# Performance work log

Hardware: AMD Instinct MI355X
Metric: run time of the kernel (lower is better)

Reference implementation:

```python
import jax, jax.numpy as jnp
import numpy as np

N, E, G, B, L = 24576, 98304, 512, 512, 1000
F_IN, H1, C1, C2, HID = 5, 2, 64, 128, 256


def setup_inputs() -> dict:
    key = jax.random.key(0)
    ks = jax.random.split(key, 20)
    rn = lambda k, s: jax.random.normal(k, s, jnp.float32) * 0.1
    return {
        "x": jax.random.normal(ks[0], (N, F_IN), jnp.float32),
        "edge_index": jax.random.randint(ks[1], (2, E), 0, N),
        "batch": jnp.sort(jax.random.randint(ks[2], (N,), 0, G)),
        "protein_seq": jax.random.randint(ks[3], (B, L), 0, 22),
        "W1": rn(ks[4], (F_IN, H1 * C1)), "att_src1": rn(ks[5], (H1, C1)), "att_dst1": rn(ks[6], (H1, C1)), "b1": jnp.zeros((H1 * C1,), jnp.float32),
        "W2": rn(ks[7], (H1 * C1, C2)), "att_src2": rn(ks[8], (1, C2)), "att_dst2": rn(ks[9], (1, C2)), "b2": jnp.zeros((C2,), jnp.float32),
        "Wd": rn(ks[10], (C2, HID)), "bd": jnp.zeros((HID,), jnp.float32),
        "Pe": rn(ks[11], (22, 64)),
        "K1": rn(ks[12], (64, 64, 3)), "bk1": jnp.zeros((64,), jnp.float32),
        "K2": rn(ks[13], (128, 64, 5)), "bk2": jnp.zeros((128,), jnp.float32),
        "Wp": rn(ks[14], (128, HID)), "bp": jnp.zeros((HID,), jnp.float32),
        "Wf1": rn(ks[15], (2 * HID, 128)), "bf1": jnp.zeros((128,), jnp.float32),
        "Wf2": rn(ks[16], (128, 64)), "bf2": jnp.zeros((64,), jnp.float32),
        "Wo": rn(ks[17], (64, 1)), "bo": jnp.zeros((1,), jnp.float32),
    }


def _gat(x, edge_index, W, att_src, att_dst, b, heads, out_ch):
    """PyG GATConv: add self-loops, per-edge LeakyReLU(0.2) scores, segment softmax over dst."""
    n = x.shape[0]
    h = (x @ W).reshape(n, heads, out_ch)
    loop = jnp.arange(n)
    src = jnp.concatenate([edge_index[0], loop])
    dst = jnp.concatenate([edge_index[1], loop])
    a_s = jnp.sum(h * att_src[None], axis=-1)  # [n, H]
    a_d = jnp.sum(h * att_dst[None], axis=-1)
    e = jax.nn.leaky_relu(a_s[src] + a_d[dst], negative_slope=0.2)  # [E+n, H]
    m = jax.ops.segment_max(e, dst, num_segments=n)
    w = jnp.exp(e - m[dst])
    den = jax.ops.segment_sum(w, dst, num_segments=n)
    alpha = w / (den[dst] + 1e-16)
    out = jax.ops.segment_sum(h[src] * alpha[..., None], dst, num_segments=n)
    return out.reshape(n, heads * out_ch) + b


def _conv1d(x, k, pad):  # x: [B,C,L], k: [O,I,K]
    return jax.lax.conv_general_dilated(x, k, (1,), [(pad, pad)], dimension_numbers=("NCH", "OIH", "NCH"))


def reference(x, edge_index, batch, protein_seq, W1, att_src1, att_dst1, b1, W2, att_src2, att_dst2, b2, Wd, bd, Pe, K1, bk1, K2, bk2, Wp, bp, Wf1, bf1, Wf2, bf2, Wo, bo):
    # drug branch (GAT x2 + global mean pool)
    g = jax.nn.elu(_gat(x, edge_index, W1, att_src1, att_dst1, b1, H1, C1))
    g = jax.nn.elu(_gat(g, edge_index, W2, att_src2, att_dst2, b2, 1, C2))
    sums = jax.ops.segment_sum(g, batch, num_segments=G)
    cnt = jax.ops.segment_sum(jnp.ones((g.shape[0], 1), g.dtype), batch, num_segments=G)
    drug = jax.nn.relu(sums / jnp.maximum(cnt, 1.0) @ Wd + bd)
    # protein branch (embed -> conv1d x2 -> global max pool)
    pe = Pe[protein_seq].transpose(0, 2, 1)  # [B, 64, L]
    p = jax.nn.elu(_conv1d(pe, K1, 1) + bk1[None, :, None])
    p = jax.nn.elu(_conv1d(p, K2, 2) + bk2[None, :, None])
    prot = jax.nn.relu(jnp.max(p, axis=2) @ Wp + bp)
    # head
    h = jnp.concatenate([drug, prot], axis=1)
    h = jax.nn.relu(h @ Wf1 + bf1)
    h = jax.nn.relu(h @ Wf2 + bf2)
    return h @ Wo + bo
```

## Files before the change

### kernel.cpp

```cpp
#include <hip/hip_runtime.h>
#include <hip/hip_bf16.h>
#include <math.h>

#define NN 24576
#define NE 98304
#define ETOT (NE + NN)
#define NG 512
#define NB 512
#define LL 1000
#define TL 124
#define NTILE 9
#define PROT_BLKS (NB * NTILE)
#define CNT_BLKS (ETOT / 256)
#define AS1_BLKS (NN * 2 / 256)

typedef __attribute__((ext_vector_type(8))) short short8;
typedef __attribute__((ext_vector_type(4))) short short4v;
typedef __attribute__((ext_vector_type(4))) float f32x4;

__device__ inline short f2bf(float x) {
    union { __hip_bfloat16 b; short s; } u;
    u.b = __float2bfloat16(x);
    return u.s;
}

__device__ inline float bf2f(short s) {
    return __uint_as_float(((unsigned)(unsigned short)s) << 16);
}

__device__ inline void atomicMaxFloat(float* addr, float val) {
    int* ai = (int*)addr;
    int old = __float_as_int(*addr);
    while (__int_as_float(old) < val) {
        int assumed = old;
        old = atomicCAS(ai, assumed, __float_as_int(val));
        if (old == assumed) break;
    }
}

__global__ void k_init_prep(int* deg, int* cursor, float* sums, float* cnt, float* pmax,
                            const float* K1, const float* K2, const float* W2, const float* Pe,
                            const float* W1, const float* as1c, const float* ad1c,
                            const float* as2c, const float* ad2c,
                            short* Bswz1, short* Bswz2, short* Bh2, short* Bl2, short* Peb,
                            float* wvec) {
    int bid = blockIdx.x, t = threadIdx.x;
    if (bid < 256) {
        int i = bid * 256 + t;
        if (i < NN) { deg[i] = 0; cursor[i] = 0; }
        if (i < NG * 128) sums[i] = 0.f;
        if (i < NG) cnt[i] = 0.f;
        if (i < NB * 128) pmax[i] = -1e30f;
        return;
    }
    int idx = (bid - 256) * 256 + t;
    if (idx < 22 * 64) Peb[idx] = f2bf(Pe[idx]);
    if (idx < 20) {
        int q = idx % 10, hd = q / 5, f = q % 5;
        const float* av = (idx < 10) ? as1c : ad1c;
        float s = 0.f;
        for (int c = 0; c < 64; c++) s += W1[f * 128 + hd * 64 + c] * av[hd * 64 + c];
        wvec[idx < 10 ? q : 10 + q] = s;
    }
    if (idx >= 32 && idx < 288) {
        int q = idx - 32;
        int kk = q & 127;
        const float* av = (q < 128) ? as2c : ad2c;
        float s = 0.f;
        for (int n2 = 0; n2 < 128; n2++) s += W2[kk * 128 + n2] * av[n2];
        wvec[idx] = s;
    }
    if (idx < 192 * 64) {
        int j = idx & 7, lane = (idx >> 3) & 63, rest = idx >> 9;
        int nt = rest & 3, kb = rest >> 2;
        int k = kb * 32 + ((lane >> 4) << 3) + j;
        int n = nt * 16 + (lane & 15);
        int kk = k >> 6, i = k & 63;
        Bswz1[idx] = f2bf(K1[n * 192 + i * 3 + kk]);
    }
    if (idx < 320 * 128) {
        int j = idx & 7, lane = (idx >> 3) & 63, rest = idx >> 9;
        int nt = rest & 7, kb = rest >> 3;
        int k = kb * 32 + ((lane >> 4) << 3) + j;
        int n = nt * 16 + (lane & 15);
        int kk = k / 64, i = k % 64;
        Bswz2[idx] = f2bf(K2[n * 320 + i * 5 + kk]);
    }
    if (idx < 128 * 128) {
        int j = idx & 7, lane = (idx >> 3) & 63, rest = idx >> 9;
        int nt = rest & 7, kb = rest >> 3;
        int k = kb * 32 + ((lane >> 4) << 3) + j;
        int n = nt * 16 + (lane & 15);
        float v = W2[k * 128 + n];
        short hh = f2bf(v);
        Bh2[idx] = hh;
        Bl2[idx] = f2bf(v - bf2f(hh));
    }
}

#define SSTR 72
__global__ __launch_bounds__(256, 4) void k_prot_cnt_as1(
    const int* seq, const short* Peb, const short* Bswz1, const float* bk1,
    const short* Bswz2, const float* bk2, float* pmax,
    const int* ei, int* deg,
    const float* x, const float* wvec, float* as1o, float* ad1o) {
    int bid = blockIdx.x;
    int t = threadIdx.x;

    if (bid >= PROT_BLKS) {
        int rb = bid - PROT_BLKS;
        if (rb < CNT_BLKS) {
            int e = rb * 256 + t;
            int d = (e < NE) ? ei[NE + e] : e - NE;
            atomicAdd(&deg[d], 1);
        } else {
            int idx = (rb - CNT_BLKS) * 256 + t;
            int n = idx >> 1, hd = idx & 1;
            float s = 0.f, dv = 0.f;
#pragma unroll
            for (int f = 0; f < 5; f++) {
                float xv = x[n * 5 + f];
                s += xv * wvec[hd * 5 + f];
                dv += xv * wvec[10 + hd * 5 + f];
            }
            as1o[idx] = s;
            ad1o[idx] = dv;
        }
        return;
    }

    __shared__ __align__(16) short sEmb[130 * SSTR];
    __shared__ __align__(16) short s1[132 * SSTR];

    int b = bid / NTILE;
    int tile = bid - b * NTILE;
    int t0 = tile * TL;
    int wv = t >> 6, lane = t & 63;
    int ln15 = lane & 15, quad = lane >> 4;
    int mhalf = wv & 1, nhalf = wv >> 1;

    for (int j0 = 0; j0 < 130; j0 += 64) {
        int j = j0 + (t >> 2);
        if (j < 130) {
            int c0 = (t & 3) * 16;
            int l = t0 - 3 + j;
            int id = (l >= 0 && l < LL) ? seq[b * LL + l] : -1;
            short* dst = &sEmb[j * SSTR + c0];
            if (id >= 0) {
                const short8* src = (const short8*)&Peb[id * 64 + c0];
                *(short8*)dst = src[0];
                *(short8*)(dst + 8) = src[1];
            } else {
                *(short8*)dst = (short8){0, 0, 0, 0, 0, 0, 0, 0};
                *(short8*)(dst + 8) = (short8){0, 0, 0, 0, 0, 0, 0, 0};
            }
        }
    }
    s1[(128 + (t >> 6)) * SSTR + (t & 63)] = 0;
    __syncthreads();

    {
        f32x4 acc[4][2];
#pragma unroll
        for (int mi = 0; mi < 4; mi++)
#pragma unroll
            for (int ni = 0; ni < 2; ni++) acc[mi][ni] = (f32x4){0.f, 0.f, 0.f, 0.f};
#pragma unroll
        for (int kb = 0; kb < 6; kb++) {
            int koff = kb * 32 + quad * 8;
            int kk = koff >> 6, i0 = koff & 63;
            short8 b0 = *(const short8*)&Bswz1[((kb * 4 + nhalf * 2 + 0) * 64 + lane) * 8];
            short8 b1 = *(const short8*)&Bswz1[((kb * 4 + nhalf * 2 + 1) * 64 + lane) * 8];
#pragma unroll
            for (int mi = 0; mi < 4; mi++) {
                int arow = (mhalf * 4 + mi) * 16 + ln15 + kk;
                short8 a = *(const short8*)&sEmb[arow * SSTR + i0];
                acc[mi][0] = __builtin_amdgcn_mfma_f32_16x16x32_bf16(a, b0, acc[mi][0], 0, 0, 0);
                acc[mi][1] = __builtin_amdgcn_mfma_f32_16x16x32_bf16(a, b1, acc[mi][1], 0, 0, 0);
            }
        }
#pragma unroll
        for (int mi = 0; mi < 4; mi++) {
            int mt = mhalf * 4 + mi;
#pragma unroll
            for (int ni = 0; ni < 2; ni++) {
                int col = (nhalf * 2 + ni) * 16 + ln15;
                float bias = bk1[col];
#pragma unroll
                for (int r = 0; r < 4; r++) {
                    int q = mt * 16 + quad * 4 + r;
                    int l = t0 - 2 + q;
                    float v = acc[mi][ni][r] + bias;
                    v = v > 0.f ? v : __expf(v) - 1.f;
                    s1[q * SSTR + col] = (l >= 0 && l < LL) ? f2bf(v) : (short)0;
                }
            }
        }
    }
    __syncthreads();

    f32x4 acc2[4][4];
#pragma unroll
    for (int mi = 0; mi < 4; mi++)
#pragma unroll
        for (int ni = 0; ni < 4; ni++) acc2[mi][ni] = (f32x4){0.f, 0.f, 0.f, 0.f};
#pragma unroll 2
    for (int kb = 0; kb < 10; kb++) {
        int koff = kb * 32 + quad * 8;
        int kk = koff >> 6, i0 = koff & 63;
        short8 a[4], bb[4];
#pragma unroll
        for (int mi = 0; mi < 4; mi++) {
            int arow = (mhalf * 4 + mi) * 16 + ln15 + kk;
            a[mi] = *(const short8*)&s1[arow * SSTR + i0];
        }
#pragma unroll
        for (int ni = 0; ni < 4; ni++)
            bb[ni] = *(const short8*)&Bswz2[((kb * 8 + nhalf * 4 + ni) * 64 + lane) * 8];
#pragma unroll
        for (int mi = 0; mi < 4; mi++)
#pragma unroll
            for (int ni = 0; ni < 4; ni++)
                acc2[mi][ni] = __builtin_amdgcn_mfma_f32_16x16x32_bf16(a[mi], bb[ni], acc2[mi][ni], 0, 0, 0);
    }

#pragma unroll
    for (int ni = 0; ni < 4; ni++) {
        int col = (nhalf * 4 + ni) * 16 + ln15;
        float mx = -1e30f;
#pragma unroll
        for (int mi = 0; mi < 4; mi++) {
#pragma unroll
            for (int r = 0; r < 4; r++) {
                int p = (mhalf * 4 + mi) * 16 + quad * 4 + r;
                if (p < TL && t0 + p < LL) mx = fmaxf(mx, acc2[mi][ni][r]);
            }
        }
        mx = fmaxf(mx, __shfl_xor(mx, 16, 64));
        mx = fmaxf(mx, __shfl_xor(mx, 32, 64));
        if (quad == 0) {
            float v = mx + bk2[col];
            v = v > 0.f ? v : __expf(v) - 1.f;
            atomicMaxFloat(&pmax[b * 128 + col], v);
        }
    }
}

__global__ void k_scan1(const int* deg, int* excl, int* part) {
    __shared__ int s[256];
    int b = blockIdx.x, t = threadIdx.x, i = b * 256 + t;
    int v = deg[i];
    s[t] = v;
    __syncthreads();
    for (int o = 1; o < 256; o <<= 1) {
        int x = (t >= o) ? s[t - o] : 0;
        __syncthreads();
        s[t] += x;
        __syncthreads();
    }
    excl[i] = s[t] - v;
    if (t == 255) part[b] = s[t];
}

__global__ void k_scan23(const int* excl, const int* part, int* rowptr) {
    __shared__ int sp[96];
    __shared__ int pref;
    int b = blockIdx.x, t = threadIdx.x;
    if (t < 96) sp[t] = part[t];
    __syncthreads();
    if (t == 0) {
        int run = 0;
        for (int i = 0; i < b; i++) run += sp[i];
        pref = run;
    }
    __syncthreads();
    int i = b * 256 + t;
    rowptr[i] = excl[i] + pref;
    if (i == 0) rowptr[NN] = ETOT;
}

__global__ void k_scatter(const int* ei, const int* rowptr, int* cursor, int* colidx) {
    int e = blockIdx.x * 256 + threadIdx.x;
    if (e >= ETOT) return;
    int s, d;
    if (e < NE) { s = ei[e]; d = ei[NE + e]; }
    else { s = d = e - NE; }
    int pos = atomicAdd(&cursor[d], 1);
    colidx[rowptr[d] + pos] = s;
}

__global__ void k_agg2x(const int* rowptr, const int* colidx, const float* x,
                        const float* as_, const float* ad_,
                        const float* W1, const float* b1, const float* wvec,
                        unsigned int* g1b, float* as2, float* ad2) {
    __shared__ float sW[640];
    __shared__ float sb1[128];
    __shared__ float swa[256];
    int t = threadIdx.x;
    for (int i = t; i < 640; i += 256) sW[i] = W1[i];
    if (t < 128) { sb1[t] = b1[t]; swa[t] = wvec[32 + t]; swa[128 + t] = wvec[160 + t]; }
    __syncthreads();

    int d = blockIdx.x * 16 + (t >> 4);
    int g = t & 15;
    int hd = (g < 5) ? 0 : 1;
    int f = (g < 5) ? g : g - 5;
    float adv = ad_[d * 2 + hd];
    int p0 = rowptr[d], p1 = rowptr[d + 1];
    float den = 0.f, acc = 0.f;
    if (g < 10) {
        for (int pc = p0; pc < p1; pc += 4) {
            int sarr[4]; float ev[4], xv[4];
#pragma unroll
            for (int i = 0; i < 4; i++) {
                int pp = pc + i;
                sarr[i] = colidx[pp < p1 ? pp : p1 - 1];
            }
#pragma unroll
            for (int i = 0; i < 4; i++) {
                ev[i] = as_[sarr[i] * 2 + hd];
                xv[i] = x[sarr[i] * 5 + f];
            }
#pragma unroll
            for (int i = 0; i < 4; i++) {
                if (pc + i < p1) {
                    float e = ev[i] + adv;
                    e = e >= 0.f ? e : 0.2f * e;
                    float w = __expf(e);
                    den += w;
                    acc += w * xv[i];
                }
            }
        }
    }
    float xn = acc / (den + 1e-16f);
    int gb = (t & 63) & ~15;
    int hcol = g >> 3;
    float xs[5];
#pragma unroll
    for (int f2 = 0; f2 < 5; f2++)
        xs[f2] = __shfl(xn, gb + hcol * 5 + f2, 64);
    float ps = 0.f, pd = 0.f;
    float g1v[8];
#pragma unroll
    for (int k = 0; k < 8; k++) {
        int col = g * 8 + k;
        float v = sb1[col];
#pragma unroll
        for (int f2 = 0; f2 < 5; f2++) v += xs[f2] * sW[f2 * 128 + col];
        v = v > 0.f ? v : __expf(v) - 1.f;
        g1v[k] = v;
        ps += v * swa[col];
        pd += v * swa[128 + col];
    }
    uint4 pk;
    pk.x = ((unsigned)(unsigned short)f2bf(g1v[1]) << 16) | (unsigned)(unsigned short)f2bf(g1v[0]);
    pk.y = ((unsigned)(unsigned short)f2bf(g1v[3]) << 16) | (unsigned)(unsigned short)f2bf(g1v[2]);
    pk.z = ((unsigned)(unsigned short)f2bf(g1v[5]) << 16) | (unsigned)(unsigned short)f2bf(g1v[4]);
    pk.w = ((unsigned)(unsigned short)f2bf(g1v[7]) << 16) | (unsigned)(unsigned short)f2bf(g1v[6]);
    *(uint4*)&g1b[d * 64 + g * 4] = pk;
#pragma unroll
    for (int msk = 1; msk < 16; msk <<= 1) {
        ps += __shfl_xor(ps, msk, 64);
        pd += __shfl_xor(pd, msk, 64);
    }
    if (g == 0) { as2[d] = ps; ad2[d] = pd; }
}

__global__ void k_agg1y(const int* rowptr, const int* colidx, const unsigned int* hb,
                        const float* as_, const float* ad_, float* yacc) {
    int t = threadIdx.x;
    int d = blockIdx.x * 4 + (t >> 6);
    int c = t & 63;
    float adv = ad_[d];
    int p0 = rowptr[d], p1 = rowptr[d + 1];
    float den = 0.f, acc0 = 0.f, acc1 = 0.f;
    for (int pc = p0; pc < p1; pc += 4) {
        int sarr[4]; float ev[4]; unsigned int hv[4];
#pragma unroll
        for (int i = 0; i < 4; i++) {
            int pp = pc + i;
            sarr[i] = colidx[pp < p1 ? pp : p1 - 1];
        }
#pragma unroll
        for (int i = 0; i < 4; i++) {
            ev[i] = as_[sarr[i]];
            hv[i] = hb[sarr[i] * 64 + c];
        }
#pragma unroll
        for (int i = 0; i < 4; i++) {
            if (pc + i < p1) {
                float e = ev[i] + adv;
                e = e >= 0.f ? e : 0.2f * e;
                float w = __expf(e);
                den += w;
                acc0 += w * __uint_as_float(hv[i] << 16);
                acc1 += w * __uint_as_float(hv[i] & 0xFFFF0000u);
            }
        }
    }
    float inv = 1.f / (den + 1e-16f);
    ((float2*)yacc)[d * 64 + c] = (float2){acc0 * inv, acc1 * inv};
}

#define ASTR 136
__global__ __launch_bounds__(256, 2) void k_g2mm(
    const float* yacc, const short* Bh, const short* Bl, const float* b2, float* g2) {
    __shared__ __align__(16) short Ah[64 * ASTR];
    __shared__ __align__(16) short Al[64 * ASTR];
    int t = threadIdx.x;
    int m0 = blockIdx.x * 64;
    int wv = t >> 6, lane = t & 63;
    int ln15 = lane & 15, quad = lane >> 4;

    for (int i = t; i < 64 * 32; i += 256) {
        int row = i >> 5, c4 = (i & 31) * 4;
        float4 v = *(const float4*)&yacc[(m0 + row) * 128 + c4];
        short4v hi, lo;
        hi.x = f2bf(v.x); lo.x = f2bf(v.x - bf2f(hi.x));
        hi.y = f2bf(v.y); lo.y = f2bf(v.y - bf2f(hi.y));
        hi.z = f2bf(v.z); lo.z = f2bf(v.z - bf2f(hi.z));
        hi.w = f2bf(v.w); lo.w = f2bf(v.w - bf2f(hi.w));
        *(short4v*)&Ah[row * ASTR + c4] = hi;
        *(short4v*)&Al[row * ASTR + c4] = lo;
    }
    __syncthreads();

    f32x4 acc[8];
#pragma unroll
    for (int nt = 0; nt < 8; nt++) acc[nt] = (f32x4){0.f, 0.f, 0.f, 0.f};
    int arow = wv * 16 + ln15;
#pragma unroll
    for (int kb = 0; kb < 4; kb++) {
        int koff = kb * 32 + quad * 8;
        short8 a_hi = *(const short8*)&Ah[arow * ASTR + koff];
        short8 a_lo = *(const short8*)&Al[arow * ASTR + koff];
#pragma unroll
        for (int nt = 0; nt < 8; nt++) {
            short8 bh = *(const short8*)&Bh[((kb * 8 + nt) * 64 + lane) * 8];
            short8 bl = *(const short8*)&Bl[((kb * 8 + nt) * 64 + lane) * 8];
            acc[nt] = __builtin_amdgcn_mfma_f32_16x16x32_bf16(a_hi, bh, acc[nt], 0, 0, 0);
            acc[nt] = __builtin_amdgcn_mfma_f32_16x16x32_bf16(a_hi, bl, acc[nt], 0, 0, 0);
            acc[nt] = __builtin_amdgcn_mfma_f32_16x16x32_bf16(a_lo, bh, acc[nt], 0, 0, 0);
        }
    }
#pragma unroll
    for (int nt = 0; nt < 8; nt++) {
        int col = nt * 16 + ln15;
        float bias = b2[col];
#pragma unroll
        for (int r = 0; r < 4; r++) {
            float v = acc[nt][r] + bias;
            v = v > 0.f ? v : __expf(v) - 1.f;
            int n = m0 + wv * 16 + quad * 4 + r;
            g2[n * 128 + col] = v;
        }
    }
}

__global__ void k_pool(const float* g2, const int* batch, float* sums, float* cnt) {
    __shared__ int sb[96];
    int blk = blockIdx.x, j = threadIdx.x;
    int n0 = blk * 96;
    if (j < 96) sb[j] = batch[n0 + j];
    __syncthreads();
    float v[4];
#pragma unroll
    for (int i = 0; i < 4; i++) v[i] = g2[(n0 + i) * 128 + j];
    int cur = sb[0], runStart = 0;
    float acc = 0.f;
    for (int q0 = 0; q0 < 96; q0 += 4) {
        float nv[4] = {0.f, 0.f, 0.f, 0.f};
        if (q0 + 4 < 96) {
#pragma unroll
            for (int i = 0; i < 4; i++) nv[i] = g2[(n0 + q0 + 4 + i) * 128 + j];
        }
#pragma unroll
        for (int i = 0; i < 4; i++) {
            int q = q0 + i;
            int bb = sb[q];
            if (bb != cur) {
                atomicAdd(&sums[cur * 128 + j], acc);
                if (j == 0) atomicAdd(&cnt[cur], (float)(q - runStart));
                cur = bb; acc = 0.f; runStart = q;
            }
            acc += v[i];
        }
#pragma unroll
        for (int i = 0; i < 4; i++) v[i] = nv[i];
    }
    atomicAdd(&sums[cur * 128 + j], acc);
    if (j == 0) atomicAdd(&cnt[cur], (float)(96 - runStart));
}

__global__ void k_tail(const float* pmax, const float* Wp, const float* bp,
                       const float* sums, const float* cnt, const float* Wd, const float* bd,
                       const float* Wf1, const float* bf1, const float* Wf2, const float* bf2,
                       const float* Wo, const float* bo, float* out) {
    __shared__ float in2[512];
    __shared__ float hh[128];
    __shared__ float h2s[64];
    int g = blockIdx.x, t = threadIdx.x;

    float pacc = bp[t];
#pragma unroll 8
    for (int i = 0; i < 128; i++) pacc += pmax[g * 128 + i] * Wp[i * 256 + t];
    in2[256 + t] = pacc > 0.f ? pacc : 0.f;

    float c = cnt[g]; c = c < 1.f ? 1.f : c;
    float inv = 1.f / c;
    float dacc = bd[t];
#pragma unroll 8
    for (int i = 0; i < 128; i++) dacc += sums[g * 128 + i] * inv * Wd[i * 256 + t];
    in2[t] = dacc > 0.f ? dacc : 0.f;
    __syncthreads();

    if (t < 128) {
        float acc = bf1[t];
#pragma unroll 8
        for (int cc = 0; cc < 512; cc++) acc += in2[cc] * Wf1[cc * 128 + t];
        hh[t] = acc > 0.f ? acc : 0.f;
    }
    __syncthreads();
    if (t < 64) {
        float a2 = bf2[t];
#pragma unroll 8
        for (int cc = 0; cc < 128; cc++) a2 += hh[cc] * Wf2[cc * 64 + t];
        h2s[t] = a2 > 0.f ? a2 : 0.f;
    }
    __syncthreads();
    if (t == 0) {
        float o = bo[0];
#pragma unroll 8
        for (int cc = 0; cc < 64; cc++) o += h2s[cc] * Wo[cc];
        out[g] = o;
    }
}

extern "C" void kernel_launch(void* const* d_in, const int* in_sizes, int n_in,
                              void* d_out, int out_size, void* d_ws, size_t ws_size,
                              hipStream_t stream) {
    (void)in_sizes; (void)n_in; (void)out_size; (void)ws_size;
    const float* x   = (const float*)d_in[0];
    const int* ei    = (const int*)d_in[1];
    const int* batch = (const int*)d_in[2];
    const int* seq   = (const int*)d_in[3];
    const float* W1  = (const float*)d_in[4];
    const float* a_s1 = (const float*)d_in[5];
    const float* a_d1 = (const float*)d_in[6];
    const float* b1  = (const float*)d_in[7];
    const float* W2  = (const float*)d_in[8];
    const float* a_s2 = (const float*)d_in[9];
    const float* a_d2 = (const float*)d_in[10];
    const float* b2  = (const float*)d_in[11];
    const float* Wd  = (const float*)d_in[12];
    const float* bd  = (const float*)d_in[13];
    const float* Pe  = (const float*)d_in[14];
    const float* K1  = (const float*)d_in[15];
    const float* bk1 = (const float*)d_in[16];
    const float* K2  = (const float*)d_in[17];
    const float* bk2 = (const float*)d_in[18];
    const float* Wp  = (const float*)d_in[19];
    const float* bp  = (const float*)d_in[20];
    const float* Wf1 = (const float*)d_in[21];
    const float* bf1 = (const float*)d_in[22];
    const float* Wf2 = (const float*)d_in[23];
    const float* bf2 = (const float*)d_in[24];
    const float* Wo  = (const float*)d_in[25];
    const float* bo  = (const float*)d_in[26];
    float* out = (float*)d_out;

    float* w = (float*)d_ws;
    float* g1bf = w; w += NN * 64;
    float* yacc = w; w += NN * 128;
    float* g2   = w; w += NN * 128;
    float* as1  = w; w += NN * 2;
    float* ad1  = w; w += NN * 2;
    float* as2  = w; w += NN;
    float* ad2  = w; w += NN;
    float* sums = w; w += NG * 128;
    float* cnt  = w; w += NG;
    float* pmax = w; w += NB * 128;
    float* wvec = w; w += 512;
    short* Bswz1 = (short*)w; w += 192 * 64 / 2;
    short* Bswz2 = (short*)w; w += 320 * 128 / 2;
    short* Bh2  = (short*)w; w += 128 * 128 / 2;
    short* Bl2  = (short*)w; w += 128 * 128 / 2;
    short* Peb  = (short*)w; w += 22 * 64 / 2 + 8;
    int* deg    = (int*)w; w += NN;
    int* cursor = (int*)w; w += NN;
    int* excl   = (int*)w; w += NN;
    int* part   = (int*)w; w += 128;
    int* rowptr = (int*)w; w += NN + 8;
    int* colidx = (int*)w; w += ETOT;

    unsigned int* g1b = (unsigned int*)g1bf;

    hipLaunchKernelGGL(k_init_prep, dim3(256 + 160), dim3(256), 0, stream,
                       deg, cursor, sums, cnt, pmax,
                       K1, K2, W2, Pe, W1, a_s1, a_d1, a_s2, a_d2,
                       Bswz1, Bswz2, Bh2, Bl2, Peb, wvec);

    hipLaunchKernelGGL(k_prot_cnt_as1, dim3(PROT_BLKS + CNT_BLKS + AS1_BLKS), dim3(256), 0, stream,
                       seq, Peb, Bswz1, bk1, Bswz2, bk2, pmax,
                       ei, deg, x, wvec, as1, ad1);

    hipLaunchKernelGGL(k_scan1, dim3(NN / 256), dim3(256), 0, stream, deg, excl, part);
    hipLaunchKernelGGL(k_scan23, dim3(NN / 256), dim3(256), 0, stream, excl, part, rowptr);
    hipLaunchKernelGGL(k_scatter, dim3(ETOT / 256), dim3(256), 0, stream, ei, rowptr, cursor, colidx);

    hipLaunchKernelGGL(k_agg2x, dim3(NN / 16), dim3(256), 0, stream,
                       rowptr, colidx, x, as1, ad1, W1, b1, wvec, g1b, as2, ad2);

    hipLaunchKernelGGL(k_agg1y, dim3(NN / 4), dim3(256), 0, stream,
                       rowptr, colidx, g1b, as2, ad2, yacc);

    hipLaunchKernelGGL(k_g2mm, dim3(NN / 64), dim3(256), 0, stream,
                       yacc, Bh2, Bl2, b2, g2);

    hipLaunchKernelGGL(k_pool, dim3(NN / 96), dim3(128), 0, stream, g2, batch, sums, cnt);

    hipLaunchKernelGGL(k_tail, dim3(NG), dim3(256), 0, stream,
                       pmax, Wp, bp, sums, cnt, Wd, bd, Wf1, bf1, Wf2, bf2, Wo, bo, out);
}
```

Measured before the change: 308.8 us.

## Split protein conv work into four slices co-scheduled with graph kernels

```diff
diff --git a/kernel.cpp b/kernel.cpp
--- a/kernel.cpp
+++ b/kernel.cpp
@@ -11,8 +11,12 @@
 #define TL 124
 #define NTILE 9
 #define PROT_BLKS (NB * NTILE)
+#define PSLICE (PROT_BLKS / 4)
 #define CNT_BLKS (ETOT / 256)
 #define AS1_BLKS (NN * 2 / 256)
+#define SSTR 72
+#define SMEM_BYTES ((130 + 132) * SSTR * 2)
+#define ASTR 136
 
 typedef __attribute__((ext_vector_type(8))) short short8;
 typedef __attribute__((ext_vector_type(4))) short short4v;
@@ -35,6 +39,124 @@
         int assumed = old;
         old = atomicCAS(ai, assumed, __float_as_int(val));
         if (old == assumed) break;
+    }
+}
+
+__device__ __forceinline__ void protein_block(
+    int pb, int t, short* sEmb, short* s1,
+    const int* seq, const short* Peb, const short* Bswz1, const float* bk1,
+    const short* Bswz2, const float* bk2, float* pmax) {
+    int b = pb / NTILE;
+    int tile = pb - b * NTILE;
+    int t0 = tile * TL;
+    int wv = t >> 6, lane = t & 63;
+    int ln15 = lane & 15, quad = lane >> 4;
+    int mhalf = wv & 1, nhalf = wv >> 1;
+
+    for (int j0 = 0; j0 < 130; j0 += 64) {
+        int j = j0 + (t >> 2);
+        if (j < 130) {
+            int c0 = (t & 3) * 16;
+            int l = t0 - 3 + j;
+            int id = (l >= 0 && l < LL) ? seq[b * LL + l] : -1;
+            short* dst = &sEmb[j * SSTR + c0];
+            if (id >= 0) {
+                const short8* src = (const short8*)&Peb[id * 64 + c0];
+                *(short8*)dst = src[0];
+                *(short8*)(dst + 8) = src[1];
+            } else {
+                *(short8*)dst = (short8){0, 0, 0, 0, 0, 0, 0, 0};
+                *(short8*)(dst + 8) = (short8){0, 0, 0, 0, 0, 0, 0, 0};
+            }
+        }
+    }
+    s1[(128 + (t >> 6)) * SSTR + (t & 63)] = 0;
+    __syncthreads();
+
+    {
+        f32x4 acc[4][2];
+#pragma unroll
+        for (int mi = 0; mi < 4; mi++)
+#pragma unroll
+            for (int ni = 0; ni < 2; ni++) acc[mi][ni] = (f32x4){0.f, 0.f, 0.f, 0.f};
+#pragma unroll
+        for (int kb = 0; kb < 6; kb++) {
+            int koff = kb * 32 + quad * 8;
+            int kk = koff >> 6, i0 = koff & 63;
+            short8 b0 = *(const short8*)&Bswz1[((kb * 4 + nhalf * 2 + 0) * 64 + lane) * 8];
+            short8 b1 = *(const short8*)&Bswz1[((kb * 4 + nhalf * 2 + 1) * 64 + lane) * 8];
+#pragma unroll
+            for (int mi = 0; mi < 4; mi++) {
+                int arow = (mhalf * 4 + mi) * 16 + ln15 + kk;
+                short8 a = *(const short8*)&sEmb[arow * SSTR + i0];
+                acc[mi][0] = __builtin_amdgcn_mfma_f32_16x16x32_bf16(a, b0, acc[mi][0], 0, 0, 0);
+                acc[mi][1] = __builtin_amdgcn_mfma_f32_16x16x32_bf16(a, b1, acc[mi][1], 0, 0, 0);
+            }
+        }
+#pragma unroll
+        for (int mi = 0; mi < 4; mi++) {
+            int mt = mhalf * 4 + mi;
+#pragma unroll
+            for (int ni = 0; ni < 2; ni++) {
+                int col = (nhalf * 2 + ni) * 16 + ln15;
+                float bias = bk1[col];
+#pragma unroll
+                for (int r = 0; r < 4; r++) {
+                    int q = mt * 16 + quad * 4 + r;
+                    int l = t0 - 2 + q;
+                    float v = acc[mi][ni][r] + bias;
+                    v = v > 0.f ? v : __expf(v) - 1.f;
+                    s1[q * SSTR + col] = (l >= 0 && l < LL) ? f2bf(v) : (short)0;
+                }
+            }
+        }
+    }
+    __syncthreads();
+
+    f32x4 acc2[4][4];
+#pragma unroll
+    for (int mi = 0; mi < 4; mi++)
+#pragma unroll
+        for (int ni = 0; ni < 4; ni++) acc2[mi][ni] = (f32x4){0.f, 0.f, 0.f, 0.f};
+#pragma unroll 2
+    for (int kb = 0; kb < 10; kb++) {
+        int koff = kb * 32 + quad * 8;
+        int kk = koff >> 6, i0 = koff & 63;
+        short8 a[4], bb[4];
+#pragma unroll
+        for (int mi = 0; mi < 4; mi++) {
+            int arow = (mhalf * 4 + mi) * 16 + ln15 + kk;
+            a[mi] = *(const short8*)&s1[arow * SSTR + i0];
+        }
+#pragma unroll
+        for (int ni = 0; ni < 4; ni++)
+            bb[ni] = *(const short8*)&Bswz2[((kb * 8 + nhalf * 4 + ni) * 64 + lane) * 8];
+#pragma unroll
+        for (int mi = 0; mi < 4; mi++)
+#pragma unroll
+            for (int ni = 0; ni < 4; ni++)
+                acc2[mi][ni] = __builtin_amdgcn_mfma_f32_16x16x32_bf16(a[mi], bb[ni], acc2[mi][ni], 0, 0, 0);
+    }
+
+#pragma unroll
+    for (int ni = 0; ni < 4; ni++) {
+        int col = (nhalf * 4 + ni) * 16 + ln15;
+        float mx = -1e30f;
+#pragma unroll
+        for (int mi = 0; mi < 4; mi++) {
+#pragma unroll
+            for (int r = 0; r < 4; r++) {
+                int p = (mhalf * 4 + mi) * 16 + quad * 4 + r;
+                if (p < TL && t0 + p < LL) mx = fmaxf(mx, acc2[mi][ni][r]);
+            }
+        }
+        mx = fmaxf(mx, __shfl_xor(mx, 16, 64));
+        mx = fmaxf(mx, __shfl_xor(mx, 32, 64));
+        if (quad == 0) {
+            float v = mx + bk2[col];
+            v = v > 0.f ? v : __expf(v) - 1.f;
+            atomicMaxFloat(&pmax[b * 128 + col], v);
+        }
     }
 }
 
@@ -98,190 +220,64 @@
     }
 }
 
-#define SSTR 72
-__global__ __launch_bounds__(256, 4) void k_prot_cnt_as1(
-    const int* seq, const short* Peb, const short* Bswz1, const float* bk1,
-    const short* Bswz2, const float* bk2, float* pmax,
-    const int* ei, int* deg,
-    const float* x, const float* wvec, float* as1o, float* ad1o) {
-    int bid = blockIdx.x;
-    int t = threadIdx.x;
-
-    if (bid >= PROT_BLKS) {
-        int rb = bid - PROT_BLKS;
-        if (rb < CNT_BLKS) {
-            int e = rb * 256 + t;
-            int d = (e < NE) ? ei[NE + e] : e - NE;
-            atomicAdd(&deg[d], 1);
-        } else {
-            int idx = (rb - CNT_BLKS) * 256 + t;
-            int n = idx >> 1, hd = idx & 1;
-            float s = 0.f, dv = 0.f;
-#pragma unroll
-            for (int f = 0; f < 5; f++) {
-                float xv = x[n * 5 + f];
-                s += xv * wvec[hd * 5 + f];
-                dv += xv * wvec[10 + hd * 5 + f];
-            }
-            as1o[idx] = s;
-            ad1o[idx] = dv;
-        }
+__global__ void k_cnt_as1(const int* ei, int* deg,
+                          const float* x, const float* wvec, float* as1o, float* ad1o) {
+    int bid = blockIdx.x, t = threadIdx.x;
+    if (bid < CNT_BLKS) {
+        int e = bid * 256 + t;
+        int d = (e < NE) ? ei[NE + e] : e - NE;
+        atomicAdd(&deg[d], 1);
         return;
     }
-
-    __shared__ __align__(16) short sEmb[130 * SSTR];
-    __shared__ __align__(16) short s1[132 * SSTR];
-
-    int b = bid / NTILE;
-    int tile = bid - b * NTILE;
-    int t0 = tile * TL;
-    int wv = t >> 6, lane = t & 63;
-    int ln15 = lane & 15, quad = lane >> 4;
-    int mhalf = wv & 1, nhalf = wv >> 1;
-
-    for (int j0 = 0; j0 < 130; j0 += 64) {
-        int j = j0 + (t >> 2);
-        if (j < 130) {
-            int c0 = (t & 3) * 16;
-            int l = t0 - 3 + j;
-            int id = (l >= 0 && l < LL) ? seq[b * LL + l] : -1;
-            short* dst = &sEmb[j * SSTR + c0];
-            if (id >= 0) {
-                const short8* src = (const short8*)&Peb[id * 64 + c0];
-                *(short8*)dst = src[0];
-                *(short8*)(dst + 8) = src[1];
-            } else {
-                *(short8*)dst = (short8){0, 0, 0, 0, 0, 0, 0, 0};
-                *(short8*)(dst + 8) = (short8){0, 0, 0, 0, 0, 0, 0, 0};
-            }
-        }
-    }
-    s1[(128 + (t >> 6)) * SSTR + (t & 63)] = 0;
-    __syncthreads();
-
-    {
-        f32x4 acc[4][2];
-#pragma unroll
-        for (int mi = 0; mi < 4; mi++)
-#pragma unroll
-            for (int ni = 0; ni < 2; ni++) acc[mi][ni] = (f32x4){0.f, 0.f, 0.f, 0.f};
-#pragma unroll
-        for (int kb = 0; kb < 6; kb++) {
-            int koff = kb * 32 + quad * 8;
-            int kk = koff >> 6, i0 = koff & 63;
-            short8 b0 = *(const short8*)&Bswz1[((kb * 4 + nhalf * 2 + 0) * 64 + lane) * 8];
-            short8 b1 = *(const short8*)&Bswz1[((kb * 4 + nhalf * 2 + 1) * 64 + lane) * 8];
-#pragma unroll
-            for (int mi = 0; mi < 4; mi++) {
-                int arow = (mhalf * 4 + mi) * 16 + ln15 + kk;
-                short8 a = *(const short8*)&sEmb[arow * SSTR + i0];
-                acc[mi][0] = __builtin_amdgcn_mfma_f32_16x16x32_bf16(a, b0, acc[mi][0], 0, 0, 0);
-                acc[mi][1] = __builtin_amdgcn_mfma_f32_16x16x32_bf16(a, b1, acc[mi][1], 0, 0, 0);
-            }
-        }
-#pragma unroll
-        for (int mi = 0; mi < 4; mi++) {
-            int mt = mhalf * 4 + mi;
-#pragma unroll
-            for (int ni = 0; ni < 2; ni++) {
-                int col = (nhalf * 2 + ni) * 16 + ln15;
-                float bias = bk1[col];
-#pragma unroll
-                for (int r = 0; r < 4; r++) {
-                    int q = mt * 16 + quad * 4 + r;
-                    int l = t0 - 2 + q;
-                    float v = acc[mi][ni][r] + bias;
-                    v = v > 0.f ? v : __expf(v) - 1.f;
-                    s1[q * SSTR + col] = (l >= 0 && l < LL) ? f2bf(v) : (short)0;
-                }
-            }
-        }
-    }
-    __syncthreads();
-
-    f32x4 acc2[4][4];
-#pragma unroll
-    for (int mi = 0; mi < 4; mi++)
-#pragma unroll
-        for (int ni = 0; ni < 4; ni++) acc2[mi][ni] = (f32x4){0.f, 0.f, 0.f, 0.f};
-#pragma unroll 2
-    for (int kb = 0; kb < 10; kb++) {
-        int koff = kb * 32 + quad * 8;
-        int kk = koff >> 6, i0 = koff & 63;
-        short8 a[4], bb[4];
-#pragma unroll
-        for (int mi = 0; mi < 4; mi++) {
-            int arow = (mhalf * 4 + mi) * 16 + ln15 + kk;
-            a[mi] = *(const short8*)&s1[arow * SSTR + i0];
-        }
-#pragma unroll
-        for (int ni = 0; ni < 4; ni++)
-            bb[ni] = *(const short8*)&Bswz2[((kb * 8 + nhalf * 4 + ni) * 64 + lane) * 8];
-#pragma unroll
-        for (int mi = 0; mi < 4; mi++)
-#pragma unroll
-            for (int ni = 0; ni < 4; ni++)
-                acc2[mi][ni] = __builtin_amdgcn_mfma_f32_16x16x32_bf16(a[mi], bb[ni], acc2[mi][ni], 0, 0, 0);
-    }
-
-#pragma unroll
-    for (int ni = 0; ni < 4; ni++) {
-        int col = (nhalf * 4 + ni) * 16 + ln15;
-        float mx = -1e30f;
-#pragma unroll
-        for (int mi = 0; mi < 4; mi++) {
-#pragma unroll
-            for (int r = 0; r < 4; r++) {
-                int p = (mhalf * 4 + mi) * 16 + quad * 4 + r;
-                if (p < TL && t0 + p < LL) mx = fmaxf(mx, acc2[mi][ni][r]);
-            }
-        }
-        mx = fmaxf(mx, __shfl_xor(mx, 16, 64));
-        mx = fmaxf(mx, __shfl_xor(mx, 32, 64));
-        if (quad == 0) {
-            float v = mx + bk2[col];
-            v = v > 0.f ? v : __expf(v) - 1.f;
-            atomicMaxFloat(&pmax[b * 128 + col], v);
-        }
-    }
-}
-
-__global__ void k_scan1(const int* deg, int* excl, int* part) {
+    int idx = (bid - CNT_BLKS) * 256 + t;
+    int n = idx >> 1, hd = idx & 1;
+    float s = 0.f, dv = 0.f;
+#pragma unroll
+    for (int f = 0; f < 5; f++) {
+        float xv = x[n * 5 + f];
+        s += xv * wvec[hd * 5 + f];
+        dv += xv * wvec[10 + hd * 5 + f];
+    }
+    as1o[idx] = s;
+    ad1o[idx] = dv;
+}
+
+__global__ void k_rowptr(const int* deg, int* rowptr) {
     __shared__ int s[256];
+    __shared__ int red[4];
     int b = blockIdx.x, t = threadIdx.x, i = b * 256 + t;
     int v = deg[i];
     s[t] = v;
     __syncthreads();
     for (int o = 1; o < 256; o <<= 1) {
-        int x = (t >= o) ? s[t - o] : 0;
+        int xx = (t >= o) ? s[t - o] : 0;
         __syncthreads();
-        s[t] += x;
+        s[t] += xx;
         __syncthreads();
     }
-    excl[i] = s[t] - v;
-    if (t == 255) part[b] = s[t];
-}
-
-__global__ void k_scan23(const int* excl, const int* part, int* rowptr) {
-    __shared__ int sp[96];
-    __shared__ int pref;
-    int b = blockIdx.x, t = threadIdx.x;
-    if (t < 96) sp[t] = part[t];
-    __syncthreads();
-    if (t == 0) {
-        int run = 0;
-        for (int i = 0; i < b; i++) run += sp[i];
-        pref = run;
-    }
-    __syncthreads();
-    int i = b * 256 + t;
-    rowptr[i] = excl[i] + pref;
+    int excl = s[t] - v;
+    int psum = 0;
+    for (int k = t; k < b * 256; k += 256) psum += deg[k];
+    for (int off = 32; off > 0; off >>= 1) psum += __shfl_down(psum, off, 64);
+    if ((t & 63) == 0) red[t >> 6] = psum;
+    __syncthreads();
+    int pref = red[0] + red[1] + red[2] + red[3];
+    rowptr[i] = excl + pref;
     if (i == 0) rowptr[NN] = ETOT;
 }
 
-__global__ void k_scatter(const int* ei, const int* rowptr, int* cursor, int* colidx) {
-    int e = blockIdx.x * 256 + threadIdx.x;
-    if (e >= ETOT) return;
+__global__ __launch_bounds__(256, 4) void k_scat_prot(
+    int pstart, const int* seq, const short* Peb, const short* Bswz1, const float* bk1,
+    const short* Bswz2, const float* bk2, float* pmax,
+    const int* ei, const int* rowptr, int* cursor, int* colidx) {
+    __shared__ __align__(16) char smem[SMEM_BYTES];
+    int bid = blockIdx.x, t = threadIdx.x;
+    if (bid < PSLICE) {
+        protein_block(pstart + bid, t, (short*)smem, (short*)(smem + 130 * SSTR * 2),
+                      seq, Peb, Bswz1, bk1, Bswz2, bk2, pmax);
+        return;
+    }
+    int e = (bid - PSLICE) * 256 + t;
     int s, d;
     if (e < NE) { s = ei[e]; d = ei[NE + e]; }
     else { s = d = e - NE; }
@@ -289,19 +285,29 @@
     colidx[rowptr[d] + pos] = s;
 }
 
-__global__ void k_agg2x(const int* rowptr, const int* colidx, const float* x,
-                        const float* as_, const float* ad_,
-                        const float* W1, const float* b1, const float* wvec,
-                        unsigned int* g1b, float* as2, float* ad2) {
-    __shared__ float sW[640];
-    __shared__ float sb1[128];
-    __shared__ float swa[256];
-    int t = threadIdx.x;
+__global__ __launch_bounds__(256, 4) void k_agg2x_prot(
+    int pstart, const int* seq, const short* Peb, const short* Bswz1, const float* bk1,
+    const short* Bswz2, const float* bk2, float* pmax,
+    const int* rowptr, const int* colidx, const float* x,
+    const float* as_, const float* ad_,
+    const float* W1, const float* b1, const float* wvec,
+    unsigned int* g1b, float* as2, float* ad2) {
+    __shared__ __align__(16) char smem[SMEM_BYTES];
+    int bid = blockIdx.x, t = threadIdx.x;
+    if (bid < PSLICE) {
+        protein_block(pstart + bid, t, (short*)smem, (short*)(smem + 130 * SSTR * 2),
+                      seq, Peb, Bswz1, bk1, Bswz2, bk2, pmax);
+        return;
+    }
+    int abid = bid - PSLICE;
+    float* sW = (float*)smem;
+    float* sb1v = sW + 640;
+    float* swa = sb1v + 128;
     for (int i = t; i < 640; i += 256) sW[i] = W1[i];
-    if (t < 128) { sb1[t] = b1[t]; swa[t] = wvec[32 + t]; swa[128 + t] = wvec[160 + t]; }
-    __syncthreads();
-
-    int d = blockIdx.x * 16 + (t >> 4);
+    if (t < 128) { sb1v[t] = b1[t]; swa[t] = wvec[32 + t]; swa[128 + t] = wvec[160 + t]; }
+    __syncthreads();
+
+    int d = abid * 16 + (t >> 4);
     int g = t & 15;
     int hd = (g < 5) ? 0 : 1;
     int f = (g < 5) ? g : g - 5;
@@ -345,7 +351,7 @@
 #pragma unroll
     for (int k = 0; k < 8; k++) {
         int col = g * 8 + k;
-        float v = sb1[col];
+        float v = sb1v[col];
 #pragma unroll
         for (int f2 = 0; f2 < 5; f2++) v += xs[f2] * sW[f2 * 128 + col];
         v = v > 0.f ? v : __expf(v) - 1.f;
@@ -403,13 +409,20 @@
     ((float2*)yacc)[d * 64 + c] = (float2){acc0 * inv, acc1 * inv};
 }
 
-#define ASTR 136
-__global__ __launch_bounds__(256, 2) void k_g2mm(
+__global__ __launch_bounds__(256, 4) void k_g2mm_prot(
+    int pstart, const int* seq, const short* Peb, const short* Bswz1, const float* bk1,
+    const short* Bswz2, const float* bk2, float* pmax,
     const float* yacc, const short* Bh, const short* Bl, const float* b2, float* g2) {
-    __shared__ __align__(16) short Ah[64 * ASTR];
-    __shared__ __align__(16) short Al[64 * ASTR];
-    int t = threadIdx.x;
-    int m0 = blockIdx.x * 64;
+    __shared__ __align__(16) char smem[SMEM_BYTES];
+    int bid = blockIdx.x, t = threadIdx.x;
+    if (bid < PSLICE) {
+        protein_block(pstart + bid, t, (short*)smem, (short*)(smem + 130 * SSTR * 2),
+                      seq, Peb, Bswz1, bk1, Bswz2, bk2, pmax);
+        return;
+    }
+    short* Ah = (short*)smem;
+    short* Al = Ah + 64 * ASTR;
+    int m0 = (bid - PSLICE) * 64;
     int wv = t >> 6, lane = t & 63;
     int ln15 = lane & 15, quad = lane >> 4;
 
@@ -458,27 +471,40 @@
     }
 }
 
-__global__ void k_pool(const float* g2, const int* batch, float* sums, float* cnt) {
-    __shared__ int sb[96];
-    int blk = blockIdx.x, j = threadIdx.x;
+__global__ __launch_bounds__(256, 4) void k_pool_prot(
+    int pstart, const int* seq, const short* Peb, const short* Bswz1, const float* bk1,
+    const short* Bswz2, const float* bk2, float* pmax,
+    const float* g2, const int* batch, float* sums, float* cnt) {
+    __shared__ __align__(16) char smem[SMEM_BYTES];
+    int bid = blockIdx.x, t = threadIdx.x;
+    if (bid < PSLICE) {
+        protein_block(pstart + bid, t, (short*)smem, (short*)(smem + 130 * SSTR * 2),
+                      seq, Peb, Bswz1, bk1, Bswz2, bk2, pmax);
+        return;
+    }
+    int* sb = (int*)smem;
+    int blk = bid - PSLICE;
+    int j = t & 127, half = t >> 7;
     int n0 = blk * 96;
-    if (j < 96) sb[j] = batch[n0 + j];
-    __syncthreads();
+    if (t < 96) sb[t] = batch[n0 + t];
+    __syncthreads();
+    int base = half * 48;
+    int nn0 = n0 + base;
     float v[4];
 #pragma unroll
-    for (int i = 0; i < 4; i++) v[i] = g2[(n0 + i) * 128 + j];
-    int cur = sb[0], runStart = 0;
+    for (int i = 0; i < 4; i++) v[i] = g2[(nn0 + i) * 128 + j];
+    int cur = sb[base], runStart = 0;
     float acc = 0.f;
-    for (int q0 = 0; q0 < 96; q0 += 4) {
+    for (int q0 = 0; q0 < 48; q0 += 4) {
         float nv[4] = {0.f, 0.f, 0.f, 0.f};
-        if (q0 + 4 < 96) {
-#pragma unroll
-            for (int i = 0; i < 4; i++) nv[i] = g2[(n0 + q0 + 4 + i) * 128 + j];
+        if (q0 + 4 < 48) {
+#pragma unroll
+            for (int i = 0; i < 4; i++) nv[i] = g2[(nn0 + q0 + 4 + i) * 128 + j];
         }
 #pragma unroll
         for (int i = 0; i < 4; i++) {
             int q = q0 + i;
-            int bb = sb[q];
+            int bb = sb[base + q];
             if (bb != cur) {
                 atomicAdd(&sums[cur * 128 + j], acc);
                 if (j == 0) atomicAdd(&cnt[cur], (float)(q - runStart));
@@ -490,7 +516,7 @@
         for (int i = 0; i < 4; i++) v[i] = nv[i];
     }
     atomicAdd(&sums[cur * 128 + j], acc);
-    if (j == 0) atomicAdd(&cnt[cur], (float)(96 - runStart));
+    if (j == 0) atomicAdd(&cnt[cur], (float)(48 - runStart));
 }
 
 __global__ void k_tail(const float* pmax, const float* Wp, const float* bp,
@@ -589,8 +615,6 @@
     short* Peb  = (short*)w; w += 22 * 64 / 2 + 8;
     int* deg    = (int*)w; w += NN;
     int* cursor = (int*)w; w += NN;
-    int* excl   = (int*)w; w += NN;
-    int* part   = (int*)w; w += 128;
     int* rowptr = (int*)w; w += NN + 8;
     int* colidx = (int*)w; w += ETOT;
 
@@ -601,24 +625,29 @@
                        K1, K2, W2, Pe, W1, a_s1, a_d1, a_s2, a_d2,
                        Bswz1, Bswz2, Bh2, Bl2, Peb, wvec);
 
-    hipLaunchKernelGGL(k_prot_cnt_as1, dim3(PROT_BLKS + CNT_BLKS + AS1_BLKS), dim3(256), 0, stream,
-                       seq, Peb, Bswz1, bk1, Bswz2, bk2, pmax,
+    hipLaunchKernelGGL(k_cnt_as1, dim3(CNT_BLKS + AS1_BLKS), dim3(256), 0, stream,
                        ei, deg, x, wvec, as1, ad1);
 
-    hipLaunchKernelGGL(k_scan1, dim3(NN / 256), dim3(256), 0, stream, deg, excl, part);
-    hipLaunchKernelGGL(k_scan23, dim3(NN / 256), dim3(256), 0, stream, excl, part, rowptr);
-    hipLaunchKernelGGL(k_scatter, dim3(ETOT / 256), dim3(256), 0, stream, ei, rowptr, cursor, colidx);
-
-    hipLaunchKernelGGL(k_agg2x, dim3(NN / 16), dim3(256), 0, stream,
+    hipLaunchKernelGGL(k_rowptr, dim3(NN / 256), dim3(256), 0, stream, deg, rowptr);
+
+    hipLaunchKernelGGL(k_scat_prot, dim3(PSLICE + ETOT / 256), dim3(256), 0, stream,
+                       0, seq, Peb, Bswz1, bk1, Bswz2, bk2, pmax,
+                       ei, rowptr, cursor, colidx);
+
+    hipLaunchKernelGGL(k_agg2x_prot, dim3(PSLICE + NN / 16), dim3(256), 0, stream,
+                       PSLICE, seq, Peb, Bswz1, bk1, Bswz2, bk2, pmax,
                        rowptr, colidx, x, as1, ad1, W1, b1, wvec, g1b, as2, ad2);
 
     hipLaunchKernelGGL(k_agg1y, dim3(NN / 4), dim3(256), 0, stream,
                        rowptr, colidx, g1b, as2, ad2, yacc);
 
-    hipLaunchKernelGGL(k_g2mm, dim3(NN / 64), dim3(256), 0, stream,
+    hipLaunchKernelGGL(k_g2mm_prot, dim3(PSLICE + NN / 64), dim3(256), 0, stream,
+                       2 * PSLICE, seq, Peb, Bswz1, bk1, Bswz2, bk2, pmax,
                        yacc, Bh2, Bl2, b2, g2);
 
-    hipLaunchKernelGGL(k_pool, dim3(NN / 96), dim3(128), 0, stream, g2, batch, sums, cnt);
+    hipLaunchKernelGGL(k_pool_prot, dim3(PSLICE + NN / 96), dim3(256), 0, stream,
+                       3 * PSLICE, seq, Peb, Bswz1, bk1, Bswz2, bk2, pmax,
+                       g2, batch, sums, cnt);
 
     hipLaunchKernelGGL(k_tail, dim3(NG), dim3(256), 0, stream,
                        pmax, Wp, bp, sums, cnt, Wd, bd, Wf1, bf1, Wf2, bf2, Wo, bo, out);
```

New measurement: 331.0 us. 7.2% more time.
